# Optimization experiments

Hardware: AMD Instinct MI355X
Metric: run time of the kernel (lower is better)

Reference implementation:

```python
import jax, jax.numpy as jnp
import numpy as np

H = 256; HID = 128; V = 50000; LV = 200
N = 512; L = 64; M = 64; C = 4; T = 8; K = 8; E = 2048


def _gru_cell(x, h, wih, whh, bih, bhh):
    gi = x @ wih.T + bih
    gh = h @ whh.T + bhh
    ir, iz, inn = jnp.split(gi, 3, -1)
    hr, hz, hn = jnp.split(gh, 3, -1)
    r = jax.nn.sigmoid(ir + hr)
    z = jax.nn.sigmoid(iz + hz)
    n = jnp.tanh(inn + r * hn)
    return (1.0 - z) * n + z * h


def _bigru(x, wih, whh, bih, bhh):
    # x: [B, L, D]; params stacked [2, ...] = (fwd, bwd). out [B, L, 2*hid]
    B = x.shape[0]
    hid = whh.shape[-1]
    def run(xseq, d):
        def step(h, xt):
            hn = _gru_cell(xt, h, wih[d], whh[d], bih[d], bhh[d])
            return hn, hn
        _, out = jax.lax.scan(step, jnp.zeros((B, hid), x.dtype), jnp.swapaxes(xseq, 0, 1))
        return jnp.swapaxes(out, 0, 1)
    fwd = run(x, 0)
    bwd = jnp.flip(run(jnp.flip(x, 1), 1), 1)
    return jnp.concatenate([fwd, bwd], -1)


def _attn_pool(x, w, b):
    # x: [..., L, H]; softmax over L (matches torch softmax(dim=0) per sequence)
    a = jnp.einsum('...lh,h->...l', x, w) + b
    wts = jax.nn.softmax(a, axis=-1)
    return jnp.einsum('...l,...lh->...h', wts, x)


def _forward(seq_emb, seq_wih, seq_whh, seq_bih, seq_bhh, seq_pw, seq_pb,
             ctx_wih, ctx_whh, ctx_bih, ctx_bhh, ctx_pw, ctx_pb,
             ast_label_tab, ast_tok_tab, ast_pw, ast_pb,
             tl_wiou, tl_biou, tl_uiou, tl_wf, tl_bf, tl_uf,
             fa_wih, fa_whh, fa_bih, fa_bhh, fa_aw, fa_ab,
             comb_w, comb_b, g1_w, g1_b, g2_w, g2_b,
             cls_w1, cls_b1, cls_w2, cls_b2,
             seq_tokens, ast_children, ast_child_mask, ast_label_ids, ast_tok_ids, ctx_nei, edges):
    n_stmt = seq_tokens.shape[1]
    # --- three sequence encoders (stmt/varname/vartype), vmapped over encoder axis
    def enc(toks, emb, wih, whh, bih, bhh, pw, pb):
        e = emb[toks]                              # [N, L, H]
        o = _bigru(e, wih, whh, bih, bhh)          # [N, L, H]
        return _attn_pool(o, pw, pb)               # [N, H]
    vecs = jax.vmap(enc)(seq_tokens, seq_emb, seq_wih, seq_whh, seq_bih, seq_bhh, seq_pw, seq_pb)
    stmt_v, varn_v, vart_v = vecs[0], vecs[1], vecs[2]
    # --- ChildSum TreeLSTM over AST, batched over statements, scanned by node index
    # (children always have lower index than parent -> valid topological order)
    tok_e = ast_tok_tab[ast_tok_ids].mean(2)       # [N, M, H]
    xn = 0.5 * ast_label_tab[ast_label_ids] + 0.5 * tok_e
    Mn = xn.shape[1]
    xs = jnp.swapaxes(xn, 0, 1)                    # [M, N, H]
    chs = jnp.swapaxes(ast_children, 0, 1)         # [M, N, C]
    cms = jnp.swapaxes(ast_child_mask, 0, 1).astype(xn.dtype)
    nidx = jnp.arange(xn.shape[0])[:, None]
    def tl_step(carry, inp):
        h_arr, c_arr = carry                       # [M, N, H] each
        m, x, ch, msk = inp
        ch_h = h_arr[ch, nidx] * msk[..., None]    # [N, C, H], masked children
        ch_c = c_arr[ch, nidx] * msk[..., None]
        h_sum = ch_h.sum(1)
        iou = x @ tl_wiou.T + tl_biou + h_sum @ tl_uiou.T
        i, o, u = jnp.split(iou, 3, -1)
        i = jax.nn.sigmoid(i); o = jax.nn.sigmoid(o); u = jnp.tanh(u)
        fg = jax.nn.sigmoid((x @ tl_wf.T + tl_bf)[:, None, :] + ch_h @ tl_uf.T)
        c = i * u + (fg * ch_c).sum(1)
        h = o * jnp.tanh(c)
        return (h_arr.at[m].set(h), c_arr.at[m].set(c)), None
    z0 = jnp.zeros((Mn, xn.shape[0], xn.shape[2]), xn.dtype)
    (h_arr, _), _ = jax.lax.scan(tl_step, (z0, z0), (jnp.arange(Mn), xs, chs, cms))
    ast_v = _attn_pool(jnp.swapaxes(h_arr, 0, 1), ast_pw, ast_pb)   # [N, H]
    # --- context encoder over neighbor statement vectors (detached in original)
    ctx_in = jax.lax.stop_gradient(stmt_v)[ctx_nei]                 # [N, K, H]
    ctx_v = _attn_pool(_bigru(ctx_in, ctx_wih, ctx_whh, ctx_bih, ctx_bhh), ctx_pw, ctx_pb)
    # --- feature attention over the 5 per-statement feature vectors
    feats = jnp.stack([stmt_v, ast_v, varn_v, vart_v, ctx_v], axis=1)  # [N, 5, H]
    o = _bigru(feats, fa_wih, fa_whh, fa_bih, fa_bhh)
    wts = jax.nn.softmax(o @ fa_aw + fa_ab, axis=-1)
    x = jnp.einsum('nl,nlh->nh', wts, feats)
    # --- neighbor-mean combine (undirected unique edges)
    e0, e1 = edges[:, 0], edges[:, 1]
    rows = jnp.concatenate([e0, e1]); srcs = jnp.concatenate([e1, e0])
    nei_sum = jax.ops.segment_sum(x[srcs], rows, num_segments=n_stmt)
    deg = jax.ops.segment_sum(jnp.ones(rows.shape[0], x.dtype), rows, num_segments=n_stmt)
    nei_mean = nei_sum / jnp.maximum(deg, 1.0)[:, None]
    x2 = jax.nn.relu(jnp.concatenate([x, nei_mean], -1) @ comb_w.T + comb_b)
    # --- 2-layer symmetric-normalized GCN (edges both directions + self loops)
    sl = jnp.arange(n_stmt)
    r2 = jnp.concatenate([e0, e1, sl]); c2 = jnp.concatenate([e1, e0, sl])
    d2 = jax.ops.segment_sum(jnp.ones(r2.shape[0], x.dtype), r2, num_segments=n_stmt)
    dis = jnp.maximum(d2, 1.0) ** -0.5
    norm = (dis[r2] * dis[c2])[:, None]
    spmm = lambda y: jax.ops.segment_sum(norm * y[c2], r2, num_segments=n_stmt)
    h1 = jax.nn.relu(spmm(x2 @ g1_w.T + g1_b))
    h2 = jax.nn.relu(spmm(h1 @ g2_w.T + g2_b))
    gvec = jnp.concatenate([h2.mean(0), h2.max(0)], -1)
    return (jax.nn.relu(gvec @ cls_w1.T + cls_b1) @ cls_w2.T + cls_b2)[0]


def setup_inputs() -> dict:
    rng = np.random.default_rng(0)
    ks = iter(jax.random.split(jax.random.key(0), 64))
    def p(shape, s=0.05):
        return jax.random.normal(next(ks), shape, dtype=jnp.float32) * s
    inp = {}
    inp['seq_tokens'] = jnp.asarray(rng.integers(0, V, (3, N, L)), jnp.int32)
    ub = np.maximum(np.arange(M), 1)
    inp['ast_children'] = jnp.asarray((rng.random((N, M, C)) * ub[None, :, None]).astype(np.int64), jnp.int32)
    inp['ast_child_mask'] = jnp.asarray((rng.random((N, M, C)) < 0.7) & (np.arange(M)[None, :, None] > 0))
    inp['ast_label_ids'] = jnp.asarray(rng.integers(0, LV, (N, M)), jnp.int32)
    inp['ast_tok_ids'] = jnp.asarray(rng.integers(0, V, (N, M, T)), jnp.int32)
    inp['ctx_nei'] = jnp.asarray(rng.integers(0, N, (N, K)), jnp.int32)
    pairs = rng.integers(0, N, (8 * E, 2))
    pairs = pairs[pairs[:, 0] < pairs[:, 1]]
    pairs = np.unique(pairs, axis=0)[:E]
    inp['edges'] = jnp.asarray(pairs, jnp.int32)
    inp['seq_emb'] = p((3, V, H)).at[:, 0].set(0.0)  # padding_idx=0
    inp['seq_wih'] = p((3, 2, 3 * HID, H)); inp['seq_whh'] = p((3, 2, 3 * HID, HID))
    inp['seq_bih'] = p((3, 2, 3 * HID)); inp['seq_bhh'] = p((3, 2, 3 * HID))
    inp['seq_pw'] = p((3, H)); inp['seq_pb'] = p((3,))
    inp['ctx_wih'] = p((2, 3 * HID, H)); inp['ctx_whh'] = p((2, 3 * HID, HID))
    inp['ctx_bih'] = p((2, 3 * HID)); inp['ctx_bhh'] = p((2, 3 * HID))
    inp['ctx_pw'] = p((H,)); inp['ctx_pb'] = p(())
    inp['ast_label_tab'] = p((LV, H)); inp['ast_tok_tab'] = p((V, H))
    inp['ast_pw'] = p((H,)); inp['ast_pb'] = p(())
    inp['tl_wiou'] = p((3 * H, H)); inp['tl_biou'] = p((3 * H,)); inp['tl_uiou'] = p((3 * H, H))
    inp['tl_wf'] = p((H, H)); inp['tl_bf'] = p((H,)); inp['tl_uf'] = p((H, H))
    inp['fa_wih'] = p((2, 3 * HID, H)); inp['fa_whh'] = p((2, 3 * HID, HID))
    inp['fa_bih'] = p((2, 3 * HID)); inp['fa_bhh'] = p((2, 3 * HID))
    inp['fa_aw'] = p((H,)); inp['fa_ab'] = p(())
    inp['comb_w'] = p((H, 2 * H)); inp['comb_b'] = p((H,))
    inp['g1_w'] = p((H, H)); inp['g1_b'] = p((H,))
    inp['g2_w'] = p((H, H)); inp['g2_b'] = p((H,))
    inp['cls_w1'] = p((H, 2 * H)); inp['cls_b1'] = p((H,))
    inp['cls_w2'] = p((1, H)); inp['cls_b2'] = p((1,))
    return inp


def reference(seq_emb, seq_wih, seq_whh, seq_bih, seq_bhh, seq_pw, seq_pb,
              ctx_wih, ctx_whh, ctx_bih, ctx_bhh, ctx_pw, ctx_pb,
              ast_label_tab, ast_tok_tab, ast_pw, ast_pb,
              tl_wiou, tl_biou, tl_uiou, tl_wf, tl_bf, tl_uf,
              fa_wih, fa_whh, fa_bih, fa_bhh, fa_aw, fa_ab,
              comb_w, comb_b, g1_w, g1_b, g2_w, g2_b,
              cls_w1, cls_b1, cls_w2, cls_b2,
              seq_tokens, ast_children, ast_child_mask, ast_label_ids, ast_tok_ids, ctx_nei, edges):
    return _forward(seq_emb, seq_wih, seq_whh, seq_bih, seq_bhh, seq_pw, seq_pb,
                    ctx_wih, ctx_whh, ctx_bih, ctx_bhh, ctx_pw, ctx_pb,
                    ast_label_tab, ast_tok_tab, ast_pw, ast_pb,
                    tl_wiou, tl_biou, tl_uiou, tl_wf, tl_bf, tl_uf,
                    fa_wih, fa_whh, fa_bih, fa_bhh, fa_aw, fa_ab,
                    comb_w, comb_b, g1_w, g1_b, g2_w, g2_b,
                    cls_w1, cls_b1, cls_w2, cls_b2,
                    seq_tokens, ast_children, ast_child_mask, ast_label_ids, ast_tok_ids, ctx_nei, edges)
```

## Files before the change

kernel.cpp:

```cpp
#include <hip/hip_runtime.h>
#include <hip/hip_bf16.h>
#include <cmath>


__device__ __forceinline__ float sigf(float x) { return 1.f / (1.f + expf(-x)); }
__device__ __forceinline__ float b2f(__hip_bfloat16 x) { return __bfloat162float(x); }
__device__ __forceinline__ float bu2f(unsigned short u) {
  union { float f; unsigned i; } v; v.i = ((unsigned)u) << 16; return v.f;
}
__device__ __forceinline__ float fsig(float x) {
  return __builtin_amdgcn_rcpf(1.f + __expf(-x));
}
__device__ __forceinline__ float ftanh(float x) {
  float cx = fminf(fmaxf(x, -15.f), 15.f);
  float e = __expf(2.f * cx);
  return 1.f - 2.f * __builtin_amdgcn_rcpf(e + 1.f);
}

typedef __attribute__((ext_vector_type(8))) short bf16x8v;
typedef __attribute__((ext_vector_type(4))) float f32x4;

__device__ __forceinline__ void gload16(const __hip_bfloat16* g, __hip_bfloat16* l) {
  __builtin_amdgcn_global_load_lds((const __attribute__((address_space(1))) void*)g,
                                   (__attribute__((address_space(3))) void*)l, 16, 0, 0);
}

__device__ __forceinline__ void lds_barrier() {
  asm volatile("s_waitcnt lgkmcnt(0)" ::: "memory");
  __builtin_amdgcn_sched_barrier(0);
  __builtin_amdgcn_s_barrier();
}

__global__ __launch_bounds__(256) void k_build_wx(const float* __restrict__ wiou,
                                                  const float* __restrict__ wf,
                                                  const float* __restrict__ biou,
                                                  const float* __restrict__ bf,
                                                  float* __restrict__ w,
                                                  float* __restrict__ b) {
  int i = blockIdx.x * 256 + threadIdx.x;
  if (i < 1024 * 256) {
    int j = i >> 8, k = i & 255;
    w[i] = (j < 768) ? wiou[j * 256 + k] : wf[(j - 768) * 256 + k];
  }
  if (i < 1024) b[i] = (i < 768) ? biou[i] : bf[i - 768];
}

__global__ __launch_bounds__(256) void k_build_wproj(const float* __restrict__ uiou,
                                                     const float* __restrict__ uf,
                                                     float* __restrict__ w) {
  int i = blockIdx.x * 256 + threadIdx.x;
  if (i >= 1024 * 256) return;
  int j = i >> 8, k = i & 255;
  w[i] = (j < 768) ? uiou[j * 256 + k] : uf[(j - 768) * 256 + k];
}

__global__ __launch_bounds__(256) void k_zero_misc(float* __restrict__ nei_sum,
                                                   int* __restrict__ deg,
                                                   int* __restrict__ flag) {
  int i = blockIdx.x * 256 + threadIdx.x;
  if (i < 512 * 256) nei_sum[i] = 0.f;
  if (i < 512) deg[i] = 0;
  if (i == 0) *flag = 0;
}

__global__ __launch_bounds__(256) void k_mask_detect(const unsigned* __restrict__ raw,
                                                     int* __restrict__ flag) {
  int i = blockIdx.x * 256 + threadIdx.x;
  if (i < 32768) {
    if (raw[i] > 1u) atomicOr(flag, 1);
  }
}

__global__ __launch_bounds__(256) void k_mask_convert(const void* __restrict__ raw,
                                                      const int* __restrict__ flag,
                                                      int* __restrict__ msk) {
  int i = blockIdx.x * 256 + threadIdx.x;
  if (i >= 512 * 64 * 4) return;
  int v;
  if (*flag) v = ((const unsigned char*)raw)[i] != 0;
  else       v = ((const int*)raw)[i] != 0;
  msk[i] = v;
}

__global__ __launch_bounds__(256) void k_cvt_bf16(const float* __restrict__ A,
                                                  const int* __restrict__ ridx,
                                                  int rstride,
                                                  __hip_bfloat16* __restrict__ out) {
  int r = blockIdx.x * 8 + (threadIdx.x >> 5);
  int k = (threadIdx.x & 31) * 8;
  const float* src = A + (size_t)(ridx ? ridx[r] : r) * rstride + k;
  float4 v0 = *(const float4*)src;
  float4 v1 = *(const float4*)(src + 4);
  union { ushort4 u; __hip_bfloat16 b[4]; } p0, p1;
  p0.b[0] = __float2bfloat16(v0.x); p0.b[1] = __float2bfloat16(v0.y);
  p0.b[2] = __float2bfloat16(v0.z); p0.b[3] = __float2bfloat16(v0.w);
  p1.b[0] = __float2bfloat16(v1.x); p1.b[1] = __float2bfloat16(v1.y);
  p1.b[2] = __float2bfloat16(v1.z); p1.b[3] = __float2bfloat16(v1.w);
  __hip_bfloat16* dst = out + (size_t)r * 256 + k;
  *(ushort4*)dst = p0.u;
  *(ushort4*)(dst + 4) = p1.u;
}

__global__ __launch_bounds__(256) void k_gemm_mfma(const __hip_bfloat16* __restrict__ A,
                                                   const __hip_bfloat16* __restrict__ W,
                                                   const float* __restrict__ bias,
                                                   void* __restrict__ Cv,
                                                   int R, int K, int J,
                                                   int relu, int out_bf16) {
  __shared__ __align__(16) __hip_bfloat16 As[128 * 32];
  __shared__ __align__(16) __hip_bfloat16 Bs[128 * 32];
  int njt = J >> 7;
  int rt = blockIdx.x / njt;
  int jt = blockIdx.x - rt * njt;
  int tid = threadIdx.x;
  int w = tid >> 6, lane = tid & 63;
  int wr = w >> 1, wc = w & 1;

  const __hip_bfloat16* ga = A + (size_t)(rt * 128 + w * 32 + (lane >> 2)) * K + (lane & 3) * 8;
  const __hip_bfloat16* gb = W + (size_t)(jt * 128 + w * 32 + (lane >> 2)) * K + (lane & 3) * 8;
  __hip_bfloat16* lA0 = As + w * 1024;
  __hip_bfloat16* lB0 = Bs + w * 1024;
  size_t gstep16 = (size_t)16 * K;

  f32x4 acc[4][4];
#pragma unroll
  for (int m = 0; m < 4; ++m)
#pragma unroll
    for (int n = 0; n < 4; ++n) acc[m][n] = (f32x4){0.f, 0.f, 0.f, 0.f};

  int fr = lane & 15;
  int kg = (lane >> 4) * 8;
  const __hip_bfloat16* raA = As + (size_t)(wr * 64 + fr) * 32 + kg;
  const __hip_bfloat16* raB = Bs + (size_t)(wc * 64 + fr) * 32 + kg;

  for (int k0 = 0; k0 < K; k0 += 32) {
    __syncthreads();
    gload16(ga, lA0);
    gload16(ga + gstep16, lA0 + 512);
    gload16(gb, lB0);
    gload16(gb + gstep16, lB0 + 512);
    ga += 32; gb += 32;
    __syncthreads();
    bf16x8v a[4], b[4];
#pragma unroll
    for (int m = 0; m < 4; ++m) a[m] = *(const bf16x8v*)(raA + m * 512);
#pragma unroll
    for (int n = 0; n < 4; ++n) b[n] = *(const bf16x8v*)(raB + n * 512);
#pragma unroll
    for (int m = 0; m < 4; ++m)
#pragma unroll
      for (int n = 0; n < 4; ++n)
        acc[m][n] = __builtin_amdgcn_mfma_f32_16x16x32_bf16(a[m], b[n], acc[m][n], 0, 0, 0);
  }

  int row0 = rt * 128 + wr * 64 + (lane >> 4) * 4;
  int col0 = jt * 128 + wc * 64 + fr;
#pragma unroll
  for (int n = 0; n < 4; ++n) {
    int col = col0 + n * 16;
    float bv = bias ? bias[col] : 0.f;
#pragma unroll
    for (int m = 0; m < 4; ++m) {
#pragma unroll
      for (int j = 0; j < 4; ++j) {
        float v = acc[m][n][j] + bv;
        if (relu) v = fmaxf(v, 0.f);
        size_t idx = (size_t)(row0 + m * 16 + j) * J + col;
        if (out_bf16) ((__hip_bfloat16*)Cv)[idx] = __float2bfloat16(v);
        else ((float*)Cv)[idx] = v;
      }
    }
  }
}

__global__ __launch_bounds__(256) void k_gemm128(const float* __restrict__ A,
                                                 const int* __restrict__ ridx,
                                                 int rstride,
                                                 const float* __restrict__ W,
                                                 const float* __restrict__ bias,
                                                 float* __restrict__ C,
                                                 int R, int K, int J, int relu,
                                                 int out_bf16) {
  __shared__ float As[16][132];
  __shared__ float Ws[16][132];
  int njt = J >> 7;
  int rt = blockIdx.x / njt;
  int jt = blockIdx.x % njt;
  int tid = threadIdx.x;
  int tx = tid & 15, ty = tid >> 4;

  int row2 = tid >> 1;
  int kq = (tid & 1) * 4;
  int gr = rt * 128 + row2;
  const float* arow = A + (size_t)(ridx ? ridx[gr] : gr) * rstride;
  const float* wrow = W + (size_t)(jt * 128 + row2) * K;

  float acc[8][8];
#pragma unroll
  for (int i = 0; i < 8; ++i)
#pragma unroll
    for (int j = 0; j < 8; ++j) acc[i][j] = 0.f;

  for (int k0 = 0; k0 < K; k0 += 16) {
    float4 av0 = *(const float4*)(arow + k0 + kq);
    float4 av1 = *(const float4*)(arow + k0 + kq + 8);
    float4 wv0 = *(const float4*)(wrow + k0 + kq);
    float4 wv1 = *(const float4*)(wrow + k0 + kq + 8);
    __syncthreads();
    As[kq + 0][row2] = av0.x; As[kq + 1][row2] = av0.y;
    As[kq + 2][row2] = av0.z; As[kq + 3][row2] = av0.w;
    As[kq + 8][row2] = av1.x; As[kq + 9][row2] = av1.y;
    As[kq + 10][row2] = av1.z; As[kq + 11][row2] = av1.w;
    Ws[kq + 0][row2] = wv0.x; Ws[kq + 1][row2] = wv0.y;
    Ws[kq + 2][row2] = wv0.z; Ws[kq + 3][row2] = wv0.w;
    Ws[kq + 8][row2] = wv1.x; Ws[kq + 9][row2] = wv1.y;
    Ws[kq + 10][row2] = wv1.z; Ws[kq + 11][row2] = wv1.w;
    __syncthreads();
#pragma unroll
    for (int kk = 0; kk < 16; ++kk) {
      float a[8], b[8];
      *(float4*)&a[0] = *(const float4*)&As[kk][ty * 4];
      *(float4*)&a[4] = *(const float4*)&As[kk][64 + ty * 4];
      *(float4*)&b[0] = *(const float4*)&Ws[kk][tx * 4];
      *(float4*)&b[4] = *(const float4*)&Ws[kk][64 + tx * 4];
#pragma unroll
      for (int i = 0; i < 8; ++i)
#pragma unroll
        for (int j = 0; j < 8; ++j) acc[i][j] += a[i] * b[j];
    }
  }

  int col0 = jt * 128 + tx * 4;
  int col1 = jt * 128 + 64 + tx * 4;
  float b0[4], b1[4];
#pragma unroll
  for (int j = 0; j < 4; ++j) {
    b0[j] = bias ? bias[col0 + j] : 0.f;
    b1[j] = bias ? bias[col1 + j] : 0.f;
  }
#pragma unroll
  for (int i = 0; i < 8; ++i) {
    int row = rt * 128 + ((i < 4) ? (ty * 4 + i) : (64 + ty * 4 + i - 4));
    float v0[4], v1[4];
#pragma unroll
    for (int j = 0; j < 4; ++j) {
      float x0 = acc[i][j] + b0[j];
      float x1 = acc[i][j + 4] + b1[j];
      if (relu) { x0 = fmaxf(x0, 0.f); x1 = fmaxf(x1, 0.f); }
      v0[j] = x0; v1[j] = x1;
    }
    if (out_bf16) {
      __hip_bfloat16* Cb = (__hip_bfloat16*)C;
      union { ushort4 u; __hip_bfloat16 b[4]; } p0, p1;
#pragma unroll
      for (int j = 0; j < 4; ++j) { p0.b[j] = __float2bfloat16(v0[j]); p1.b[j] = __float2bfloat16(v1[j]); }
      *(ushort4*)(Cb + (size_t)row * J + col0) = p0.u;
      *(ushort4*)(Cb + (size_t)row * J + col1) = p1.u;
    } else {
      *(float4*)(C + (size_t)row * J + col0) = *(float4*)v0;
      *(float4*)(C + (size_t)row * J + col1) = *(float4*)v1;
    }
  }
}

__global__ __launch_bounds__(512) void k_gru5(const __hip_bfloat16* __restrict__ gi,
                                              const __hip_bfloat16* __restrict__ whhb,
                                              const float* __restrict__ bhh,
                                              float* __restrict__ out,
                                              int L, int bpe,
                                              unsigned gi_se, unsigned whh_se,
                                              unsigned bhh_se, unsigned out_se) {
  __shared__ __align__(16) __hip_bfloat16 hsb[16][136];
  __shared__ float outl[16][396];
  int tid = threadIdx.x;
  int d = blockIdx.y;
  int e = blockIdx.x / bpe;
  int n0 = (blockIdx.x - e * bpe) * 16;
  gi += (size_t)e * gi_se;
  whhb += (size_t)e * whh_se;
  bhh += (size_t)e * bhh_se;
  out += (size_t)e * out_se;

  int w = tid >> 6, lane = tid & 63;
  int fr = lane & 15;
  int kg = (lane >> 4) * 8;
  int jw = w * 48;

  bf16x8v bfr[3][4];
  const __hip_bfloat16* wb = whhb + (size_t)d * 384 * 128;
#pragma unroll
  for (int cf = 0; cf < 3; ++cf)
#pragma unroll
    for (int kf = 0; kf < 4; ++kf)
      bfr[cf][kf] = *(const bf16x8v*)(wb + (size_t)(jw + cf * 16 + fr) * 128 + kf * 32 + kg);

  int s = tid >> 5;
  int j0 = (tid & 31) * 4;
  const float* bh = bhh + d * 384;
  float4 br = *(const float4*)(bh + j0);
  float4 bz = *(const float4*)(bh + 128 + j0);
  float4 bn = *(const float4*)(bh + 256 + j0);

  float h[4] = {0.f, 0.f, 0.f, 0.f};
  for (int i = tid; i < 16 * 136; i += 512) ((__hip_bfloat16*)hsb)[i] = __float2bfloat16(0.f);
  __syncthreads();

  int t = d ? (L - 1) : 0;
  int dt = d ? -1 : 1;
  const __hip_bfloat16* gbase = gi + (size_t)(n0 + s) * L * 768 + d * 384 + j0;

  const __hip_bfloat16* g0 = gbase + (size_t)t * 768;
  ushort4 cr = *(const ushort4*)g0;
  ushort4 cz = *(const ushort4*)(g0 + 128);
  ushort4 cn4 = *(const ushort4*)(g0 + 256);

  for (int step = 0; step < L; ++step) {
    int tn = t + dt;
    tn = (tn < 0) ? 0 : ((tn >= L) ? (L - 1) : tn);
    const __hip_bfloat16* gn_ = gbase + (size_t)tn * 768;
    ushort4 nr = *(const ushort4*)gn_;
    ushort4 nz = *(const ushort4*)(gn_ + 128);
    ushort4 nn4 = *(const ushort4*)(gn_ + 256);

    f32x4 acc[3];
#pragma unroll
    for (int cf = 0; cf < 3; ++cf) acc[cf] = (f32x4){0.f, 0.f, 0.f, 0.f};
#pragma unroll
    for (int kf = 0; kf < 4; ++kf) {
      bf16x8v a = *(const bf16x8v*)(&hsb[fr][kf * 32 + kg]);
#pragma unroll
      for (int cf = 0; cf < 3; ++cf)
        acc[cf] = __builtin_amdgcn_mfma_f32_16x16x32_bf16(a, bfr[cf][kf], acc[cf], 0, 0, 0);
    }
    int r0 = (lane >> 4) * 4;
#pragma unroll
    for (int cf = 0; cf < 3; ++cf) {
      int col = jw + cf * 16 + fr;
#pragma unroll
      for (int r = 0; r < 4; ++r) outl[r0 + r][col] = acc[cf][r];
    }
    lds_barrier();

    float4 sr = *(const float4*)&outl[s][j0];
    float4 sz = *(const float4*)&outl[s][128 + j0];
    float4 sn = *(const float4*)&outl[s][256 + j0];
    float grv[4] = {bu2f(cr.x), bu2f(cr.y), bu2f(cr.z), bu2f(cr.w)};
    float gzv[4] = {bu2f(cz.x), bu2f(cz.y), bu2f(cz.z), bu2f(cz.w)};
    float gnv[4] = {bu2f(cn4.x), bu2f(cn4.y), bu2f(cn4.z), bu2f(cn4.w)};
    float srv[4] = {sr.x, sr.y, sr.z, sr.w};
    float szv[4] = {sz.x, sz.y, sz.z, sz.w};
    float snv[4] = {sn.x, sn.y, sn.z, sn.w};
    float brv[4] = {br.x, br.y, br.z, br.w};
    float bzv[4] = {bz.x, bz.y, bz.z, bz.w};
    float bnv[4] = {bn.x, bn.y, bn.z, bn.w};
#pragma unroll
    for (int j = 0; j < 4; ++j) {
      float r = fsig(grv[j] + srv[j] + brv[j]);
      float z = fsig(gzv[j] + szv[j] + bzv[j]);
      float nn = ftanh(gnv[j] + r * (snv[j] + bnv[j]));
      h[j] = (1.f - z) * nn + z * h[j];
    }
    *(float4*)(out + (size_t)((n0 + s) * L + t) * 256 + d * 128 + j0) =
        (float4){h[0], h[1], h[2], h[3]};
    union { ushort4 u; __hip_bfloat16 b[4]; } hp;
#pragma unroll
    for (int j = 0; j < 4; ++j) hp.b[j] = __float2bfloat16(h[j]);
    *(ushort4*)&hsb[s][j0] = hp.u;
    lds_barrier();

    cr = nr; cz = nz; cn4 = nn4;
    t += dt;
  }
}

__global__ __launch_bounds__(256) void k_attn_pool(const float* __restrict__ score_src,
                                                   int s_ns, int s_ls,
                                                   const float* __restrict__ val_src,
                                                   int v_ns, int v_ls,
                                                   const float* __restrict__ w,
                                                   const float* __restrict__ bptr,
                                                   float* __restrict__ dst,
                                                   int dst_stride, int L) {
  __shared__ float wts[64];
  int n = blockIdx.x;
  int tid = threadIdx.x;
  if (tid < 64) {
    float a = -INFINITY;
    if (tid < L) {
      const float* row = score_src + (size_t)n * s_ns + (size_t)tid * s_ls;
      float s = bptr[0];
      for (int h = 0; h < 256; h += 4) {
        float4 v = *(const float4*)(row + h);
        float4 wv = *(const float4*)(w + h);
        s += v.x * wv.x + v.y * wv.y + v.z * wv.z + v.w * wv.w;
      }
      a = s;
    }
    float mx = a;
#pragma unroll
    for (int off = 32; off; off >>= 1) mx = fmaxf(mx, __shfl_xor(mx, off));
    float e = (tid < L) ? expf(a - mx) : 0.f;
    float ss = e;
#pragma unroll
    for (int off = 32; off; off >>= 1) ss += __shfl_xor(ss, off);
    if (tid < L) wts[tid] = e / ss;
  }
  __syncthreads();
  float acc = 0.f;
  for (int l = 0; l < L; ++l)
    acc += wts[l] * val_src[(size_t)n * v_ns + (size_t)l * v_ls + tid];
  dst[(size_t)n * dst_stride + tid] = acc;
}

__global__ __launch_bounds__(256) void k_xn_bf16(const float* __restrict__ label_tab,
                                                 const float* __restrict__ tok_tab,
                                                 const int* __restrict__ lbl_ids,
                                                 const int* __restrict__ tok_ids,
                                                 __hip_bfloat16* __restrict__ xnb) {
  int nm = blockIdx.x;
  int h = threadIdx.x;
  const int* tids = tok_ids + (size_t)nm * 8;
  float s = 0.f;
#pragma unroll
  for (int t = 0; t < 8; ++t) s += tok_tab[(size_t)tids[t] * 256 + h];
  float v = 0.5f * label_tab[(size_t)lbl_ids[nm] * 256 + h] + 0.0625f * s;
  xnb[(size_t)nm * 256 + h] = __float2bfloat16(v);
}

__global__ __launch_bounds__(256) void k_tl_combine4(const __hip_bfloat16* __restrict__ HU,
                                                     const __hip_bfloat16* __restrict__ XWALL,
                                                     const int* __restrict__ ch,
                                                     const int* __restrict__ msk,
                                                     float* __restrict__ h_arr,
                                                     float* __restrict__ c_arr,
                                                     __hip_bfloat16* __restrict__ hbf,
                                                     int m) {
  int n = blockIdx.x, h = threadIdx.x;
  const __hip_bfloat16* xw = XWALL + ((size_t)(n * 64 + m)) * 1024;
  float si = b2f(xw[h]), so = b2f(xw[256 + h]), su = b2f(xw[512 + h]);
  float xfv = b2f(xw[768 + h]);
  const int* chp = ch + ((size_t)(n * 64 + m)) * 4;
  const int* mkp = msk + ((size_t)(n * 64 + m)) * 4;
  float cs = 0.f;
#pragma unroll
  for (int c = 0; c < 4; ++c) {
    if (mkp[c]) {
      int cc = chp[c];
      const __hip_bfloat16* hu = HU + ((size_t)cc * 512 + n) * 1024;
      si += b2f(hu[h]);
      so += b2f(hu[256 + h]);
      su += b2f(hu[512 + h]);
      float fg = fsig(xfv + b2f(hu[768 + h]));
      cs += fg * c_arr[((size_t)cc * 512 + n) * 256 + h];
    }
  }
  float iv = fsig(si), ov = fsig(so), uv = ftanh(su);
  float cn = iv * uv + cs;
  float hn = ov * ftanh(cn);
  h_arr[((size_t)m * 512 + n) * 256 + h] = hn;
  c_arr[((size_t)m * 512 + n) * 256 + h] = cn;
  hbf[(size_t)n * 256 + h] = __float2bfloat16(hn);
}

__global__ __launch_bounds__(256) void k_edge_deg(const int* __restrict__ edges,
                                                  int* __restrict__ deg, int E) {
  int i = blockIdx.x * 256 + threadIdx.x;
  if (i < E) {
    atomicAdd(&deg[edges[2 * i]], 1);
    atomicAdd(&deg[edges[2 * i + 1]], 1);
  }
}

__global__ __launch_bounds__(256) void k_nei(const int* __restrict__ edges,
                                             const float* __restrict__ x,
                                             float* __restrict__ nei_sum) {
  int e = blockIdx.x, h = threadIdx.x;
  int a = edges[2 * e], b = edges[2 * e + 1];
  atomicAdd(&nei_sum[(size_t)a * 256 + h], x[(size_t)b * 256 + h]);
  atomicAdd(&nei_sum[(size_t)b * 256 + h], x[(size_t)a * 256 + h]);
}

__global__ __launch_bounds__(256) void k_xcat(const float* __restrict__ x,
                                              const float* __restrict__ nei_sum,
                                              const int* __restrict__ deg,
                                              float* __restrict__ xcat) {
  int n = blockIdx.x, h = threadIdx.x;
  xcat[(size_t)n * 512 + h] = x[(size_t)n * 256 + h];
  float d = fmaxf((float)deg[n], 1.f);
  xcat[(size_t)n * 512 + 256 + h] = nei_sum[(size_t)n * 256 + h] / d;
}

__global__ __launch_bounds__(256) void k_spmm_self(const float* __restrict__ y,
                                                   const int* __restrict__ deg,
                                                   float* __restrict__ ob) {
  int n = blockIdx.x, h = threadIdx.x;
  float dis2 = 1.f / (float)(deg[n] + 1);
  ob[(size_t)n * 256 + h] = dis2 * y[(size_t)n * 256 + h];
}

__global__ __launch_bounds__(256) void k_spmm_edge(const float* __restrict__ y,
                                                   const int* __restrict__ deg,
                                                   const int* __restrict__ edges,
                                                   float* __restrict__ ob) {
  int e = blockIdx.x, h = threadIdx.x;
  int a = edges[2 * e], b = edges[2 * e + 1];
  float w = (1.f / sqrtf((float)(deg[a] + 1))) * (1.f / sqrtf((float)(deg[b] + 1)));
  atomicAdd(&ob[(size_t)a * 256 + h], w * y[(size_t)b * 256 + h]);
  atomicAdd(&ob[(size_t)b * 256 + h], w * y[(size_t)a * 256 + h]);
}

__global__ __launch_bounds__(256) void k_relu_inplace(float* __restrict__ p) {
  int i = blockIdx.x * 256 + threadIdx.x;
  p[i] = fmaxf(p[i], 0.f);
}

__global__ __launch_bounds__(256) void k_final(const float* __restrict__ h2,
                                               const float* __restrict__ w1,
                                               const float* __restrict__ b1,
                                               const float* __restrict__ w2,
                                               const float* __restrict__ b2,
                                               float* __restrict__ outp) {
  __shared__ float gv[512];
  __shared__ float zz[256];
  int tid = threadIdx.x;
  float mn = 0.f, mx = -INFINITY;
  for (int n = 0; n < 512; ++n) {
    float v = h2[(size_t)n * 256 + tid];
    mn += v;
    mx = fmaxf(mx, v);
  }
  gv[tid] = mn / 512.f;
  gv[256 + tid] = mx;
  __syncthreads();
  float acc = b1[tid];
  for (int k = 0; k < 512; ++k) acc += gv[k] * w1[(size_t)tid * 512 + k];
  zz[tid] = fmaxf(acc, 0.f) * w2[tid];
  __syncthreads();
  for (int s = 128; s; s >>= 1) {
    if (tid < s) zz[tid] += zz[tid + s];
    __syncthreads();
  }
  if (tid == 0) outp[0] = zz[0] + b2[0];
}

extern "C" void kernel_launch(void* const* d_in, const int* in_sizes, int n_in,
                              void* d_out, int out_size, void* d_ws, size_t ws_size,
                              hipStream_t stream) {
  const int* seq_tokens    = (const int*)d_in[0];
  const int* ast_children  = (const int*)d_in[1];
  const void* ast_mask_raw = (const void*)d_in[2];
  const int* ast_label_ids = (const int*)d_in[3];
  const int* ast_tok_ids   = (const int*)d_in[4];
  const int* ctx_nei       = (const int*)d_in[5];
  const int* edges         = (const int*)d_in[6];
  const float* seq_emb  = (const float*)d_in[7];
  const float* seq_wih  = (const float*)d_in[8];
  const float* seq_whh  = (const float*)d_in[9];
  const float* seq_bih  = (const float*)d_in[10];
  const float* seq_bhh  = (const float*)d_in[11];
  const float* seq_pw   = (const float*)d_in[12];
  const float* seq_pb   = (const float*)d_in[13];
  const float* ctx_wih  = (const float*)d_in[14];
  const float* ctx_whh  = (const float*)d_in[15];
  const float* ctx_bih  = (const float*)d_in[16];
  const float* ctx_bhh  = (const float*)d_in[17];
  const float* ctx_pw   = (const float*)d_in[18];
  const float* ctx_pb   = (const float*)d_in[19];
  const float* ast_label_tab = (const float*)d_in[20];
  const float* ast_tok_tab   = (const float*)d_in[21];
  const float* ast_pw   = (const float*)d_in[22];
  const float* ast_pb   = (const float*)d_in[23];
  const float* tl_wiou  = (const float*)d_in[24];
  const float* tl_biou  = (const float*)d_in[25];
  const float* tl_uiou  = (const float*)d_in[26];
  const float* tl_wf    = (const float*)d_in[27];
  const float* tl_bf    = (const float*)d_in[28];
  const float* tl_uf    = (const float*)d_in[29];
  const float* fa_wih   = (const float*)d_in[30];
  const float* fa_whh   = (const float*)d_in[31];
  const float* fa_bih   = (const float*)d_in[32];
  const float* fa_bhh   = (const float*)d_in[33];
  const float* fa_aw    = (const float*)d_in[34];
  const float* fa_ab    = (const float*)d_in[35];
  const float* comb_w   = (const float*)d_in[36];
  const float* comb_b   = (const float*)d_in[37];
  const float* g1_w     = (const float*)d_in[38];
  const float* g1_b     = (const float*)d_in[39];
  const float* g2_w     = (const float*)d_in[40];
  const float* g2_b     = (const float*)d_in[41];
  const float* cls_w1   = (const float*)d_in[42];
  const float* cls_b1   = (const float*)d_in[43];
  const float* cls_w2   = (const float*)d_in[44];
  const float* cls_b2   = (const float*)d_in[45];
  float* outp = (float*)d_out;
  float* ws = (float*)d_ws;
  int E = in_sizes[6] / 2;

  size_t off = 0;
  auto take = [&](size_t n) { size_t o = off; off += n; return o; };
  const size_t F_FEATS = take(512 * 5 * 256);
  const size_t F_X     = take(512 * 256);
  const size_t F_X2    = take(512 * 256);
  const size_t F_Y     = take(512 * 256);
  const size_t F_H1    = take(512 * 256);
  const size_t F_H2    = take(512 * 256);
  const size_t F_XCAT  = take(512 * 512);
  const size_t F_NEI   = take(512 * 256);
  const size_t F_DEG   = take(512);
  const size_t F_FLAG  = take(16);
  const size_t F_MSK   = take(512 * 64 * 4);
  const size_t F_WXW   = take(1024 * 256);
  const size_t F_WXB   = take(1024);
  const size_t F_WPROJ = take(1024 * 256);
  const size_t F_REGION = take(83886080);
  (void)ws_size;

  float* FEATS = ws + F_FEATS;
  float* X     = ws + F_X;
  float* X2    = ws + F_X2;
  float* Y     = ws + F_Y;
  float* H1    = ws + F_H1;
  float* H2    = ws + F_H2;
  float* XCAT  = ws + F_XCAT;
  float* NEI   = ws + F_NEI;
  int*   DEG   = (int*)(ws + F_DEG);
  int*   FLAG  = (int*)(ws + F_FLAG);
  int*   MSK   = (int*)(ws + F_MSK);
  float* WXW   = ws + F_WXW;
  float* WXB   = ws + F_WXB;
  float* WPROJ = ws + F_WPROJ;
  float* REG   = ws + F_REGION;

  __hip_bfloat16* GI3  = (__hip_bfloat16*)REG;
  float* OUT3 = REG + 38000000;
  __hip_bfloat16* XWALL16 = (__hip_bfloat16*)REG;
  float* HARR  = REG + 17000000;
  float* CARR  = REG + 25500000;
  __hip_bfloat16* HU16 = (__hip_bfloat16*)(REG + 34000000);
  __hip_bfloat16* GIFA16 = (__hip_bfloat16*)REG;
  float* OUTFA = OUT3;

  float* SCR = REG + 63500000;
  __hip_bfloat16* ABF      = (__hip_bfloat16*)(SCR);
  __hip_bfloat16* WSEQBF   = (__hip_bfloat16*)(SCR + 4200000);
  __hip_bfloat16* WCTXBF   = (__hip_bfloat16*)(SCR + 4500000);
  __hip_bfloat16* WFABF    = (__hip_bfloat16*)(SCR + 4600000);
  __hip_bfloat16* WXWBF    = (__hip_bfloat16*)(SCR + 4700000);
  __hip_bfloat16* WPROJBF  = (__hip_bfloat16*)(SCR + 4850000);
  __hip_bfloat16* HBF      = (__hip_bfloat16*)(SCR + 5000000);
  __hip_bfloat16* WHHSEQBF = (__hip_bfloat16*)(SCR + 5100000);
  __hip_bfloat16* WHHCTXBF = (__hip_bfloat16*)(SCR + 5260000);
  __hip_bfloat16* WHHFABF  = (__hip_bfloat16*)(SCR + 5320000);

  auto gemm = [&](const float* A, const int* ridx, int rstride, const float* W,
                  const float* bias, float* C, int R, int K, int J, int relu,
                  int obf) {
    dim3 g((R / 128) * (J / 128));
    k_gemm128<<<g, 256, 0, stream>>>(A, ridx, rstride, W, bias, C, R, K, J, relu, obf);
  };
  auto cvt = [&](const float* A, const int* ridx, int rstride,
                 __hip_bfloat16* ob, int R) {
    k_cvt_bf16<<<R / 8, 256, 0, stream>>>(A, ridx, rstride, ob);
  };
  auto mgemm = [&](const __hip_bfloat16* A, const __hip_bfloat16* W,
                   const float* bias, void* C, int R, int K, int J, int relu,
                   int obf) {
    dim3 g((R / 128) * (J / 128));
    k_gemm_mfma<<<g, 256, 0, stream>>>(A, W, bias, C, R, K, J, relu, obf);
  };

  k_build_wx<<<1024, 256, 0, stream>>>(tl_wiou, tl_wf, tl_biou, tl_bf, WXW, WXB);
  k_build_wproj<<<1024, 256, 0, stream>>>(tl_uiou, tl_uf, WPROJ);
  k_zero_misc<<<512, 256, 0, stream>>>(NEI, DEG, FLAG);
  k_mask_detect<<<128, 256, 0, stream>>>((const unsigned*)ast_mask_raw, FLAG);
  k_mask_convert<<<512, 256, 0, stream>>>(ast_mask_raw, FLAG, MSK);
  cvt(seq_wih, nullptr, 256, WSEQBF, 2304);
  cvt(ctx_wih, nullptr, 256, WCTXBF, 768);
  cvt(fa_wih, nullptr, 256, WFABF, 768);
  cvt(WXW, nullptr, 256, WXWBF, 1024);
  cvt(WPROJ, nullptr, 256, WPROJBF, 1024);
  cvt(seq_whh, nullptr, 256, WHHSEQBF, 1152);
  cvt(ctx_whh, nullptr, 256, WHHCTXBF, 384);
  cvt(fa_whh, nullptr, 256, WHHFABF, 384);

  const int slot_of[3] = {0, 2, 3};
  for (int e = 0; e < 3; ++e) {
    cvt(seq_emb + (size_t)e * 50000 * 256, seq_tokens + (size_t)e * 32768, 256,
        ABF, 32768);
    mgemm(ABF, WSEQBF + (size_t)e * 768 * 256, seq_bih + (size_t)e * 768,
          GI3 + (size_t)e * 32768 * 768, 32768, 256, 768, 0, 1);
  }
  k_gru5<<<dim3(96, 2), 512, 0, stream>>>(GI3, WHHSEQBF, seq_bhh, OUT3, 64, 32,
                                          32768u * 768u, 2u * 384u * 128u, 768u,
                                          32768u * 256u);
  for (int e = 0; e < 3; ++e) {
    k_attn_pool<<<512, 256, 0, stream>>>(OUT3 + (size_t)e * 32768 * 256, 64 * 256, 256,
                                         OUT3 + (size_t)e * 32768 * 256, 64 * 256, 256,
                                         seq_pw + e * 256, seq_pb + e,
                                         FEATS + slot_of[e] * 256, 1280, 64);
  }

  cvt(FEATS, ctx_nei, 1280, ABF, 4096);
  mgemm(ABF, WCTXBF, ctx_bih, GI3, 4096, 256, 768, 0, 1);
  k_gru5<<<dim3(32, 2), 512, 0, stream>>>(GI3, WHHCTXBF, ctx_bhh, OUT3, 8, 32,
                                          0, 0, 0, 0);
  k_attn_pool<<<512, 256, 0, stream>>>(OUT3, 8 * 256, 256, OUT3, 8 * 256, 256,
                                       ctx_pw, ctx_pb, FEATS + 4 * 256, 1280, 8);

  k_xn_bf16<<<32768, 256, 0, stream>>>(ast_label_tab, ast_tok_tab, ast_label_ids,
                                       ast_tok_ids, ABF);
  mgemm(ABF, WXWBF, WXB, XWALL16, 32768, 256, 1024, 0, 1);
  for (int m = 0; m < 64; ++m) {
    k_tl_combine4<<<512, 256, 0, stream>>>(HU16, XWALL16, ast_children, MSK,
                                           HARR, CARR, HBF, m);
    if (m < 63)
      mgemm(HBF, WPROJBF, nullptr, HU16 + (size_t)m * 512 * 1024,
            512, 256, 1024, 0, 1);
  }
  k_attn_pool<<<512, 256, 0, stream>>>(HARR, 256, 512 * 256, HARR, 256, 512 * 256,
                                       ast_pw, ast_pb, FEATS + 1 * 256, 1280, 64);

  cvt(FEATS, nullptr, 256, ABF, 2560);
  mgemm(ABF, WFABF, fa_bih, GIFA16, 2560, 256, 768, 0, 1);
  k_gru5<<<dim3(32, 2), 512, 0, stream>>>(GIFA16, WHHFABF, fa_bhh, OUTFA, 5, 32,
                                          0, 0, 0, 0);
  k_attn_pool<<<512, 256, 0, stream>>>(OUTFA, 5 * 256, 256, FEATS, 1280, 256,
                                       fa_aw, fa_ab, X, 256, 5);

  k_edge_deg<<<(E + 255) / 256, 256, 0, stream>>>(edges, DEG, E);
  k_nei<<<E, 256, 0, stream>>>(edges, X, NEI);
  k_xcat<<<512, 256, 0, stream>>>(X, NEI, DEG, XCAT);
  gemm(XCAT, nullptr, 512, comb_w, comb_b, X2, 512, 512, 256, 1, 0);
  gemm(X2, nullptr, 256, g1_w, g1_b, Y, 512, 256, 256, 0, 0);
  k_spmm_self<<<512, 256, 0, stream>>>(Y, DEG, H1);
  k_spmm_edge<<<E, 256, 0, stream>>>(Y, DEG, edges, H1);
  k_relu_inplace<<<512, 256, 0, stream>>>(H1);
  gemm(H1, nullptr, 256, g2_w, g2_b, Y, 512, 256, 256, 0, 0);
  k_spmm_self<<<512, 256, 0, stream>>>(Y, DEG, H2);
  k_spmm_edge<<<E, 256, 0, stream>>>(Y, DEG, edges, H2);
  k_relu_inplace<<<512, 256, 0, stream>>>(H2);
  k_final<<<1, 256, 0, stream>>>(H2, cls_w1, cls_b1, cls_w2, cls_b2, outp);
}
```

Before: 1.838 ms.

## Fuse TreeLSTM node loop into one persistent kernel with in-block MFMA projection

```diff
diff --git a/kernel.cpp b/kernel.cpp
--- a/kernel.cpp
+++ b/kernel.cpp
@@ -427,39 +427,123 @@
   xnb[(size_t)nm * 256 + h] = __float2bfloat16(v);
 }
 
-__global__ __launch_bounds__(256) void k_tl_combine4(const __hip_bfloat16* __restrict__ HU,
-                                                     const __hip_bfloat16* __restrict__ XWALL,
-                                                     const int* __restrict__ ch,
-                                                     const int* __restrict__ msk,
-                                                     float* __restrict__ h_arr,
-                                                     float* __restrict__ c_arr,
-                                                     __hip_bfloat16* __restrict__ hbf,
-                                                     int m) {
-  int n = blockIdx.x, h = threadIdx.x;
-  const __hip_bfloat16* xw = XWALL + ((size_t)(n * 64 + m)) * 1024;
-  float si = b2f(xw[h]), so = b2f(xw[256 + h]), su = b2f(xw[512 + h]);
-  float xfv = b2f(xw[768 + h]);
-  const int* chp = ch + ((size_t)(n * 64 + m)) * 4;
-  const int* mkp = msk + ((size_t)(n * 64 + m)) * 4;
-  float cs = 0.f;
-#pragma unroll
-  for (int c = 0; c < 4; ++c) {
-    if (mkp[c]) {
-      int cc = chp[c];
-      const __hip_bfloat16* hu = HU + ((size_t)cc * 512 + n) * 1024;
-      si += b2f(hu[h]);
-      so += b2f(hu[256 + h]);
-      su += b2f(hu[512 + h]);
-      float fg = fsig(xfv + b2f(hu[768 + h]));
-      cs += fg * c_arr[((size_t)cc * 512 + n) * 256 + h];
-    }
-  }
-  float iv = fsig(si), ov = fsig(so), uv = ftanh(su);
-  float cn = iv * uv + cs;
-  float hn = ov * ftanh(cn);
-  h_arr[((size_t)m * 512 + n) * 256 + h] = hn;
-  c_arr[((size_t)m * 512 + n) * 256 + h] = cn;
-  hbf[(size_t)n * 256 + h] = __float2bfloat16(hn);
+__global__ __launch_bounds__(512) void k_tl_fused(const __hip_bfloat16* __restrict__ XWALL,
+                                                  const __hip_bfloat16* __restrict__ WPROJB,
+                                                  const int* __restrict__ ch,
+                                                  const int* __restrict__ msk,
+                                                  __hip_bfloat16* __restrict__ HU,
+                                                  float* __restrict__ h_arr,
+                                                  float* __restrict__ c_arr) {
+  __shared__ __align__(16) __hip_bfloat16 hsld[16][264];
+  int tid = threadIdx.x;
+  int n0 = blockIdx.x * 16;
+  int w = tid >> 6, lane = tid & 63;
+  int fr = lane & 15;
+  int kg = (lane >> 4) * 8;
+  int s = tid >> 5;
+  int j0 = (tid & 31) * 8;
+  int n = n0 + s;
+
+  const __hip_bfloat16* wp = WPROJB + (size_t)(w * 128 + fr) * 256 + kg;
+
+  const __hip_bfloat16* xw0 = XWALL + ((size_t)n * 64 + 0) * 1024 + j0;
+  bf16x8v cxi = *(const bf16x8v*)(xw0);
+  bf16x8v cxo = *(const bf16x8v*)(xw0 + 256);
+  bf16x8v cxu = *(const bf16x8v*)(xw0 + 512);
+  bf16x8v cxf = *(const bf16x8v*)(xw0 + 768);
+  int4 cch = *(const int4*)(ch + (size_t)n * 256);
+  int4 cmk = *(const int4*)(msk + (size_t)n * 256);
+
+  for (int m = 0; m < 64; ++m) {
+    float vi[8], vo[8], vu[8], xf[8], cs[8];
+#pragma unroll
+    for (int j = 0; j < 8; ++j) {
+      vi[j] = bu2f((unsigned short)cxi[j]);
+      vo[j] = bu2f((unsigned short)cxo[j]);
+      vu[j] = bu2f((unsigned short)cxu[j]);
+      xf[j] = bu2f((unsigned short)cxf[j]);
+      cs[j] = 0.f;
+    }
+    int chv[4] = {cch.x, cch.y, cch.z, cch.w};
+    int mkv[4] = {cmk.x, cmk.y, cmk.z, cmk.w};
+#pragma unroll
+    for (int c = 0; c < 4; ++c) {
+      if (mkv[c]) {
+        int cc = chv[c];
+        const __hip_bfloat16* hu = HU + ((size_t)cc * 512 + n) * 1024 + j0;
+        bf16x8v hi = *(const bf16x8v*)(hu);
+        bf16x8v ho = *(const bf16x8v*)(hu + 256);
+        bf16x8v hn = *(const bf16x8v*)(hu + 512);
+        bf16x8v hf = *(const bf16x8v*)(hu + 768);
+        const float* cb = c_arr + ((size_t)cc * 512 + n) * 256 + j0;
+        float4 c0 = *(const float4*)(cb);
+        float4 c1 = *(const float4*)(cb + 4);
+        float cv[8] = {c0.x, c0.y, c0.z, c0.w, c1.x, c1.y, c1.z, c1.w};
+#pragma unroll
+        for (int j = 0; j < 8; ++j) {
+          vi[j] += bu2f((unsigned short)hi[j]);
+          vo[j] += bu2f((unsigned short)ho[j]);
+          vu[j] += bu2f((unsigned short)hn[j]);
+          float fg = fsig(xf[j] + bu2f((unsigned short)hf[j]));
+          cs[j] += fg * cv[j];
+        }
+      }
+    }
+    float hv[8], cnv[8];
+#pragma unroll
+    for (int j = 0; j < 8; ++j) {
+      float iv = fsig(vi[j]), ov = fsig(vo[j]), uv = ftanh(vu[j]);
+      float cn = iv * uv + cs[j];
+      cnv[j] = cn;
+      hv[j] = ov * ftanh(cn);
+    }
+    float* hb = h_arr + ((size_t)m * 512 + n) * 256 + j0;
+    float* cb2 = c_arr + ((size_t)m * 512 + n) * 256 + j0;
+    *(float4*)(hb)     = (float4){hv[0], hv[1], hv[2], hv[3]};
+    *(float4*)(hb + 4) = (float4){hv[4], hv[5], hv[6], hv[7]};
+    *(float4*)(cb2)     = (float4){cnv[0], cnv[1], cnv[2], cnv[3]};
+    *(float4*)(cb2 + 4) = (float4){cnv[4], cnv[5], cnv[6], cnv[7]};
+    union { ushort4 u[2]; __hip_bfloat16 b[8]; } hp;
+#pragma unroll
+    for (int j = 0; j < 8; ++j) hp.b[j] = __float2bfloat16(hv[j]);
+    *(ushort4*)(&hsld[s][j0]) = hp.u[0];
+    *(ushort4*)(&hsld[s][j0 + 4]) = hp.u[1];
+    lds_barrier();
+
+    int mn_ = (m < 63) ? m + 1 : 63;
+    const __hip_bfloat16* xwn = XWALL + ((size_t)n * 64 + mn_) * 1024 + j0;
+    bf16x8v nxi = *(const bf16x8v*)(xwn);
+    bf16x8v nxo = *(const bf16x8v*)(xwn + 256);
+    bf16x8v nxu = *(const bf16x8v*)(xwn + 512);
+    bf16x8v nxf = *(const bf16x8v*)(xwn + 768);
+    int4 nch = *(const int4*)(ch + ((size_t)n * 64 + mn_) * 4);
+    int4 nmk = *(const int4*)(msk + ((size_t)n * 64 + mn_) * 4);
+
+    f32x4 acc[8];
+#pragma unroll
+    for (int cf = 0; cf < 8; ++cf) acc[cf] = (f32x4){0.f, 0.f, 0.f, 0.f};
+#pragma unroll
+    for (int kf = 0; kf < 8; ++kf) {
+      bf16x8v a = *(const bf16x8v*)(&hsld[fr][kf * 32 + kg]);
+#pragma unroll
+      for (int cf = 0; cf < 8; ++cf) {
+        bf16x8v b = *(const bf16x8v*)(wp + (size_t)cf * 4096 + kf * 32);
+        acc[cf] = __builtin_amdgcn_mfma_f32_16x16x32_bf16(a, b, acc[cf], 0, 0, 0);
+      }
+    }
+    int r0 = (lane >> 4) * 4;
+    __hip_bfloat16* hub = HU + ((size_t)m * 512 + n0) * 1024 + w * 128 + fr;
+#pragma unroll
+    for (int cf = 0; cf < 8; ++cf) {
+#pragma unroll
+      for (int r = 0; r < 4; ++r)
+        hub[(size_t)(r0 + r) * 1024 + cf * 16] = __float2bfloat16(acc[cf][r]);
+    }
+    __syncthreads();
+
+    cxi = nxi; cxo = nxo; cxu = nxu; cxf = nxf;
+    cch = nch; cmk = nmk;
+  }
 }
 
 __global__ __launch_bounds__(256) void k_edge_deg(const int* __restrict__ edges,
@@ -647,7 +731,6 @@
   __hip_bfloat16* WFABF    = (__hip_bfloat16*)(SCR + 4600000);
   __hip_bfloat16* WXWBF    = (__hip_bfloat16*)(SCR + 4700000);
   __hip_bfloat16* WPROJBF  = (__hip_bfloat16*)(SCR + 4850000);
-  __hip_bfloat16* HBF      = (__hip_bfloat16*)(SCR + 5000000);
   __hip_bfloat16* WHHSEQBF = (__hip_bfloat16*)(SCR + 5100000);
   __hip_bfloat16* WHHCTXBF = (__hip_bfloat16*)(SCR + 5260000);
   __hip_bfloat16* WHHFABF  = (__hip_bfloat16*)(SCR + 5320000);
@@ -710,13 +793,8 @@
   k_xn_bf16<<<32768, 256, 0, stream>>>(ast_label_tab, ast_tok_tab, ast_label_ids,
                                        ast_tok_ids, ABF);
   mgemm(ABF, WXWBF, WXB, XWALL16, 32768, 256, 1024, 0, 1);
-  for (int m = 0; m < 64; ++m) {
-    k_tl_combine4<<<512, 256, 0, stream>>>(HU16, XWALL16, ast_children, MSK,
-                                           HARR, CARR, HBF, m);
-    if (m < 63)
-      mgemm(HBF, WPROJBF, nullptr, HU16 + (size_t)m * 512 * 1024,
-            512, 256, 1024, 0, 1);
-  }
+  k_tl_fused<<<32, 512, 0, stream>>>(XWALL16, WPROJBF, ast_children, MSK,
+                                     HU16, HARR, CARR);
   k_attn_pool<<<512, 256, 0, stream>>>(HARR, 256, 512 * 256, HARR, 256, 512 * 256,
                                        ast_pw, ast_pb, FEATS + 1 * 256, 1280, 64);
 
```

New measurement: 2.183 ms. 1.19x slower.
